# Performance work log

Measured on AMD Instinct MI355X. Metric: run time of the kernel, lower is better.

Reference implementation:

```python
import jax, jax.numpy as jnp
import numpy as np

DIM = 2048
B = 8192
RED = 16
FREQ = DIM // 2 + 1  # 1025


def setup_inputs() -> dict:
    key = jax.random.key(0)
    ks = jax.random.split(key, 8)
    s = 1.0 / np.sqrt(DIM)
    return {
        "x": jax.random.normal(ks[0], (B, DIM), dtype=jnp.float32),
        "W_in": jax.random.uniform(ks[1], (DIM, DIM), jnp.float32, -s, s),
        "b_in": jax.random.uniform(ks[2], (DIM,), jnp.float32, -s, s),
        "W_out": jax.random.uniform(ks[3], (DIM, DIM), jnp.float32, -s, s),
        "b_out": jax.random.uniform(ks[4], (DIM,), jnp.float32, -s, s),
        "freq_gate": jax.random.normal(ks[5], (FREQ, 2), dtype=jnp.float32) * 0.02,
        "W_fc1": jax.random.uniform(ks[6], (2 * DIM, DIM // RED), jnp.float32, -1.0 / np.sqrt(2 * DIM), 1.0 / np.sqrt(2 * DIM)),
        "W_fc2": jax.random.uniform(ks[7], (DIM // RED, DIM), jnp.float32, -1.0 / np.sqrt(DIM // RED), 1.0 / np.sqrt(DIM // RED)),
    }


def reference(x, W_in, b_in, W_out, b_out, freq_gate, W_fc1, W_fc2):
    # proj_in
    h = x @ W_in + b_in                      # [B, C]
    # FFT along feature dim, complex gating, inverse FFT
    hf = jnp.fft.rfft(h, axis=1)             # [B, C//2+1] complex
    gate = freq_gate[:, 0] + 1j * freq_gate[:, 1]
    hf = hf * gate[: hf.shape[1]]
    ht = jnp.fft.irfft(hf, n=h.shape[1], axis=1).astype(h.dtype)  # [B, C]
    # ChannelAttention on a 1x1 spatial map: both pools are identity
    # (original code uses AdaptiveAvgPool2d for BOTH avg and max branches)
    y = jnp.concatenate([ht, ht], axis=1)     # [B, 2C]
    y = jax.nn.relu(y @ W_fc1)                # [B, C//16]
    y = jax.nn.sigmoid(y @ W_fc2)             # [B, C]
    ht = ht * y
    # proj_out
    return ht @ W_out + b_out
```

## Files before the change

kernel.cpp:

```cpp
#include <hip/hip_runtime.h>

typedef unsigned short ushort_t;
typedef unsigned int uint_t;
typedef __attribute__((ext_vector_type(8))) short short8;
typedef __attribute__((ext_vector_type(4))) float f32x4;

#define DIM 2048
#define BATCH 8192

__device__ __forceinline__ ushort_t f2bf(float f) {
  union { float f; uint_t u; } x; x.f = f;
  uint_t r = x.u + 0x7fffu + ((x.u >> 16) & 1u);
  return (ushort_t)(r >> 16);
}
__device__ __forceinline__ float bf2f(ushort_t h) {
  union { uint_t u; float f; } x; x.u = ((uint_t)h) << 16; return x.f;
}

__device__ __forceinline__ void gload_lds16(const void* g, void* l) {
  typedef __attribute__((address_space(1))) const unsigned int gu32;
  typedef __attribute__((address_space(3))) unsigned int lu32;
  __builtin_amdgcn_global_load_lds((gu32*)g, (lu32*)l, 16, 0, 0);
}

__device__ __forceinline__ float block_reduce_sum(float v) {
  #pragma unroll
  for (int off = 32; off; off >>= 1) v += __shfl_down(v, off);
  __shared__ float red[4];
  int t = threadIdx.x;
  if ((t & 63) == 0) red[t >> 6] = v;
  __syncthreads();
  return red[0] + red[1] + red[2] + red[3];
}

__global__ void k_c(const float* __restrict__ fg, float* __restrict__ c) {
  int n = blockIdx.x;
  int t = threadIdx.x;
  float s = 0.f;
  for (int k = 1 + t; k < 1024; k += 256) {
    int r = (k * n) & 2047;
    float sn, cs;
    sincospif((float)r * (1.0f / 1024.0f), &sn, &cs);
    s += fg[2 * k] * cs - fg[2 * k + 1] * sn;
  }
  float tot = block_reduce_sum(s);
  if (t == 0) {
    float v = fg[0] + ((n & 1) ? -fg[2048] : fg[2048]) + 2.f * tot;
    c[n] = v * (1.0f / 2048.0f);
  }
}

__global__ void k_b1(const float* __restrict__ b_in, const float* __restrict__ c,
                     float* __restrict__ b1) {
  int n = blockIdx.x;
  int t = threadIdx.x;
  float s = 0.f;
  for (int m = t; m < 2048; m += 256) s += b_in[m] * c[(n - m) & 2047];
  float tot = block_reduce_sum(s);
  if (t == 0) b1[n] = tot;
}

__global__ void k_gt(const float* __restrict__ c, uint_t* __restrict__ gt) {
  int idx = blockIdx.x * 256 + threadIdx.x;
  int r = idx >> 10;
  int c2 = (idx & 1023) << 1;
  uint_t v0 = f2bf(c[(r - c2) & 2047]);
  uint_t v1 = f2bf(c[(r - c2 - 1) & 2047]);
  gt[idx] = v0 | (v1 << 16);
}

__global__ void k_cast4(const float* __restrict__ in, ushort_t* __restrict__ out) {
  long i = (long)blockIdx.x * 256 + threadIdx.x;
  float4 v = ((const float4*)in)[i];
  ushort4 o;
  o.x = f2bf(v.x); o.y = f2bf(v.y); o.z = f2bf(v.z); o.w = f2bf(v.w);
  ((ushort4*)out)[i] = o;
}

__global__ void k_tc(const float* __restrict__ in, ushort_t* __restrict__ out,
                     int R, int C) {
  __shared__ float tile[32][33];
  int bc = blockIdx.x * 32;
  int br = blockIdx.y * 32;
  int tx = threadIdx.x, ty = threadIdx.y;
  #pragma unroll
  for (int i = ty; i < 32; i += 8)
    tile[i][tx] = in[(size_t)(br + i) * C + bc + tx];
  __syncthreads();
  #pragma unroll
  for (int i = ty; i < 32; i += 8)
    out[(size_t)(bc + i) * R + br + tx] = f2bf(tile[tx][i]);
}

__global__ void k_fc1fold(const float* __restrict__ w, ushort_t* __restrict__ out) {
  int idx = blockIdx.x * 256 + threadIdx.x;
  int j = idx >> 11;
  int m = idx & 2047;
  out[idx] = f2bf(w[(size_t)m * 128 + j] + w[(size_t)(m + 2048) * 128 + j]);
}

template <int EPI>
__launch_bounds__(256, 2)
__global__ void gemm_bt(const ushort_t* __restrict__ A, const ushort_t* __restrict__ BT,
                        void* __restrict__ C, const float* __restrict__ bias,
                        const ushort_t* __restrict__ aux, int M, int N, int K) {
  __shared__ ushort_t ldsA[128 * 32];
  __shared__ ushort_t ldsB[128 * 32];
  const int t = threadIdx.x;
  const int wave = t >> 6, lane = t & 63;
  const int bm = blockIdx.x, bn = blockIdx.y;
  const int wr = wave >> 1, wc = wave & 1;
  const int lrow = lane & 15, lk = lane >> 4;

  f32x4 acc[4][4] = {};

  const size_t arow0 = (size_t)bm * 128;
  const size_t brow0 = (size_t)bn * 128;

  for (int k0 = 0; k0 < K; k0 += 32) {
    if (k0) __syncthreads();
    #pragma unroll
    for (int h = 0; h < 2; ++h) {
      int q = t + h * 256;
      int row = q >> 2, slot = q & 3;
      int kc = slot ^ ((row >> 1) & 3);
      const ushort_t* ga = A + (arow0 + row) * K + k0 + kc * 8;
      gload_lds16(ga, &ldsA[(wave * 64 + h * 256) * 8]);
      const ushort_t* gb = BT + (brow0 + row) * K + k0 + kc * 8;
      gload_lds16(gb, &ldsB[(wave * 64 + h * 256) * 8]);
    }
    __syncthreads();

    short8 af[4], bfr[4];
    #pragma unroll
    for (int m = 0; m < 4; ++m) {
      int row = wr * 64 + m * 16 + lrow;
      int slot = lk ^ ((row >> 1) & 3);
      af[m] = *(const short8*)&ldsA[row * 32 + slot * 8];
      int rowb = wc * 64 + m * 16 + lrow;
      int slotb = lk ^ ((rowb >> 1) & 3);
      bfr[m] = *(const short8*)&ldsB[rowb * 32 + slotb * 8];
    }
    #pragma unroll
    for (int m = 0; m < 4; ++m)
      #pragma unroll
      for (int n = 0; n < 4; ++n)
        acc[m][n] = __builtin_amdgcn_mfma_f32_16x16x32_bf16(af[m], bfr[n], acc[m][n], 0, 0, 0);
  }

  const int rbase = bm * 128 + wr * 64;
  const int cbase = bn * 128 + wc * 64;
  #pragma unroll
  for (int m = 0; m < 4; ++m) {
    #pragma unroll
    for (int n = 0; n < 4; ++n) {
      int col = cbase + n * 16 + lrow;
      int row0 = rbase + m * 16 + lk * 4;
      #pragma unroll
      for (int j = 0; j < 4; ++j) {
        int r = row0 + j;
        float v = acc[m][n][j];
        size_t off = (size_t)r * N + col;
        if constexpr (EPI == 0) {
          ((ushort_t*)C)[off] = f2bf(v);
        } else if constexpr (EPI == 1) {
          ((ushort_t*)C)[off] = f2bf(v + bias[col]);
        } else if constexpr (EPI == 2) {
          ((ushort_t*)C)[off] = f2bf(v > 0.f ? v : 0.f);
        } else if constexpr (EPI == 3) {
          float y = 1.f / (1.f + __expf(-v));
          ((ushort_t*)C)[off] = f2bf(bf2f(aux[off]) * y);
        } else {
          ((float*)C)[off] = v + bias[col];
        }
      }
    }
  }
}

extern "C" void kernel_launch(void* const* d_in, const int* in_sizes, int n_in,
                              void* d_out, int out_size, void* d_ws, size_t ws_size,
                              hipStream_t stream) {
  const float* x     = (const float*)d_in[0];
  const float* W_in  = (const float*)d_in[1];
  const float* b_in  = (const float*)d_in[2];
  const float* W_out = (const float*)d_in[3];
  const float* b_out = (const float*)d_in[4];
  const float* fg    = (const float*)d_in[5];
  const float* W_fc1 = (const float*)d_in[6];
  const float* W_fc2 = (const float*)d_in[7];

  char* ws = (char*)d_ws;
  float*    c_buf  = (float*)(ws + 0);
  float*    b1     = (float*)(ws + 8192);
  ushort_t* WinBf  = (ushort_t*)(ws + 16384);
  ushort_t* W1T    = (ushort_t*)(ws + 8404992);
  ushort_t* WoutT  = (ushort_t*)(ws + 16793600);
  ushort_t* Wfc1eT = (ushort_t*)(ws + 25182208);
  ushort_t* Wfc2T  = (ushort_t*)(ws + 25706496);
  ushort_t* x_bf   = (ushort_t*)(ws + 26230784);
  ushort_t* ht_bf  = (ushort_t*)(ws + 59785216);
  ushort_t* a_bf   = (ushort_t*)(ws + 93339648);
  ushort_t* GT     = (ushort_t*)(ws + 95436800);
  ushort_t* g_bf   = (ushort_t*)(ws + 95436800);
  (void)ws_size; (void)in_sizes; (void)n_in; (void)out_size;

  k_c<<<2048, 256, 0, stream>>>(fg, c_buf);
  k_b1<<<2048, 256, 0, stream>>>(b_in, c_buf, b1);
  k_gt<<<8192, 256, 0, stream>>>(c_buf, (uint_t*)GT);
  k_cast4<<<16384, 256, 0, stream>>>(x, x_bf);
  k_cast4<<<4096, 256, 0, stream>>>(W_in, WinBf);
  k_tc<<<dim3(64, 64), dim3(32, 8), 0, stream>>>(W_out, WoutT, 2048, 2048);
  k_tc<<<dim3(64, 4), dim3(32, 8), 0, stream>>>(W_fc2, Wfc2T, 128, 2048);
  k_fc1fold<<<1024, 256, 0, stream>>>(W_fc1, Wfc1eT);

  gemm_bt<0><<<dim3(16, 16), 256, 0, stream>>>(GT, WinBf, W1T, nullptr, nullptr,
                                               2048, 2048, 2048);
  gemm_bt<1><<<dim3(64, 16), 256, 0, stream>>>(x_bf, W1T, ht_bf, b1, nullptr,
                                               8192, 2048, 2048);
  gemm_bt<2><<<dim3(64, 1), 256, 0, stream>>>(ht_bf, Wfc1eT, a_bf, nullptr, nullptr,
                                              8192, 128, 2048);
  gemm_bt<3><<<dim3(64, 16), 256, 0, stream>>>(a_bf, Wfc2T, g_bf, nullptr, ht_bf,
                                               8192, 2048, 128);
  gemm_bt<4><<<dim3(64, 16), 256, 0, stream>>>(g_bf, WoutT, (float*)d_out, b_out, nullptr,
                                               8192, 2048, 2048);
}
```

Baseline: 433.1 us.

## Use pipelined 256x256 GEMM for big projections and split-K for fc1

```diff
diff --git a/kernel.cpp b/kernel.cpp
--- a/kernel.cpp
+++ b/kernel.cpp
@@ -97,6 +97,12 @@
   int j = idx >> 11;
   int m = idx & 2047;
   out[idx] = f2bf(w[(size_t)m * 128 + j] + w[(size_t)(m + 2048) * 128 + j]);
+}
+
+__global__ void k_red4relu(const float* __restrict__ p, ushort_t* __restrict__ out) {
+  int i = blockIdx.x * 256 + threadIdx.x;
+  float s = p[i] + p[i + 1048576] + p[i + 2097152] + p[i + 3145728];
+  out[i] = f2bf(s > 0.f ? s : 0.f);
 }
 
 template <int EPI>
@@ -117,8 +123,11 @@
   const size_t arow0 = (size_t)bm * 128;
   const size_t brow0 = (size_t)bn * 128;
 
-  for (int k0 = 0; k0 < K; k0 += 32) {
-    if (k0) __syncthreads();
+  int kb = 0, ke = K;
+  if constexpr (EPI == 5) { int ks = K >> 2; kb = blockIdx.z * ks; ke = kb + ks; }
+
+  for (int k0 = kb; k0 < ke; k0 += 32) {
+    if (k0 != kb) __syncthreads();
     #pragma unroll
     for (int h = 0; h < 2; ++h) {
       int q = t + h * 256;
@@ -170,9 +179,146 @@
         } else if constexpr (EPI == 3) {
           float y = 1.f / (1.f + __expf(-v));
           ((ushort_t*)C)[off] = f2bf(bf2f(aux[off]) * y);
+        } else if constexpr (EPI == 4) {
+          ((float*)C)[off] = v + bias[col];
         } else {
-          ((float*)C)[off] = v + bias[col];
+          ((float*)C)[off + (size_t)blockIdx.z * ((size_t)M * N)] = v;
         }
+      }
+    }
+  }
+}
+
+__device__ __forceinline__ void stage_half(const ushort_t* __restrict__ src, size_t gr0,
+                                           int k0b, int ksb, char* ldsHalf, int t) {
+  #pragma unroll
+  for (int l = 0; l < 2; ++l) {
+    int o = (l * 512 + t) * 16;
+    int s = o ^ (((o >> 9) & 1) << 5);
+    int row = s >> 7, cbyte = s & 127;
+    const char* g = (const char*)src + (gr0 + row) * (size_t)ksb + k0b + cbyte;
+    char* dst = ldsHalf + (l * 512 + (t & ~63)) * 16;
+    gload_lds16(g, dst);
+  }
+}
+
+__device__ __forceinline__ short8 ldfrag(const char* regionBase, int R, int kk, int lk) {
+  int r = R & 127, h = R >> 7;
+  int lin = r * 128 + kk * 64 + lk * 16;
+  int sw = lin ^ (((lin >> 9) & 1) << 5);
+  return *(const short8*)(regionBase + h * 16384 + sw);
+}
+
+template <int EPI>
+__launch_bounds__(512, 2)
+__global__ void gemm256(const ushort_t* __restrict__ A, const ushort_t* __restrict__ BT,
+                        void* __restrict__ C, const float* __restrict__ bias,
+                        int N, int K, int nbn) {
+  __shared__ __align__(16) char L[131072];
+  const int t = threadIdx.x;
+  const int lane = t & 63, wave = t >> 6;
+  const int wm = wave >> 2, wn = wave & 3;
+  const int lrow = lane & 15, lk = lane >> 4;
+
+  int d = blockIdx.x;
+  int cpx = gridDim.x >> 3;
+  int wg = (d & 7) * cpx + (d >> 3);
+  const int bm = wg / nbn, bn = wg % nbn;
+
+  const size_t am0 = (size_t)bm * 256;
+  const size_t bn0 = (size_t)bn * 256;
+  const int ksb = K * 2;
+  const int NT = K >> 6;
+
+  f32x4 acc[8][4] = {};
+
+  stage_half(A,  am0,       0,   ksb, L + 0,             t);
+  stage_half(A,  am0 + 128, 0,   ksb, L + 16384,         t);
+  stage_half(BT, bn0,       0,   ksb, L + 32768,         t);
+  stage_half(BT, bn0 + 128, 0,   ksb, L + 49152,         t);
+  stage_half(BT, bn0,       128, ksb, L + 65536 + 32768, t);
+  stage_half(BT, bn0 + 128, 128, ksb, L + 65536 + 49152, t);
+  asm volatile("s_waitcnt vmcnt(4)" ::: "memory");
+  __builtin_amdgcn_s_barrier();
+
+  short8 bfrag[4][2];
+  short8 afrag[2][2];
+
+  for (int T = 0; T < NT; T += 2) {
+    int k1 = ((T + 1 < NT) ? T + 1 : NT - 1) * 128;
+    int k2 = ((T + 2 < NT) ? T + 2 : NT - 1) * 128;
+    int k3 = ((T + 3 < NT) ? T + 3 : NT - 1) * 128;
+    #pragma unroll
+    for (int ph = 0; ph < 8; ++ph) {
+      const int cb = ph >> 2;
+      const int cp = ph & 3;
+      const char* Ab = L + cb * 65536;
+      const char* Bb = L + cb * 65536 + 32768;
+      if (cp == 0) {
+        #pragma unroll
+        for (int n = 0; n < 4; ++n)
+          #pragma unroll
+          for (int kk = 0; kk < 2; ++kk)
+            bfrag[n][kk] = ldfrag(Bb, wn * 64 + n * 16 + lrow, kk, lk);
+      }
+      #pragma unroll
+      for (int mi = 0; mi < 2; ++mi)
+        #pragma unroll
+        for (int kk = 0; kk < 2; ++kk)
+          afrag[mi][kk] = ldfrag(Ab, wm * 128 + (cp * 2 + mi) * 16 + lrow, kk, lk);
+
+      if (ph == 0) {
+        stage_half(A, am0,       k1, ksb, L + 65536,         t);
+        stage_half(A, am0 + 128, k1, ksb, L + 65536 + 16384, t);
+      } else if (ph == 1) {
+        stage_half(BT, bn0,       k2, ksb, L + 32768, t);
+      } else if (ph == 2) {
+        stage_half(BT, bn0 + 128, k2, ksb, L + 49152, t);
+      } else if (ph == 3) {
+        asm volatile("s_waitcnt vmcnt(4)" ::: "memory");
+      } else if (ph == 4) {
+        stage_half(A, am0,       k2, ksb, L + 0,     t);
+      } else if (ph == 5) {
+        stage_half(A, am0 + 128, k2, ksb, L + 16384, t);
+      } else if (ph == 6) {
+        stage_half(BT, bn0,       k3, ksb, L + 65536 + 32768, t);
+      } else {
+        stage_half(BT, bn0 + 128, k3, ksb, L + 65536 + 49152, t);
+        asm volatile("s_waitcnt vmcnt(4)" ::: "memory");
+      }
+
+      __builtin_amdgcn_s_barrier();
+      asm volatile("s_waitcnt lgkmcnt(0)" ::: "memory");
+      __builtin_amdgcn_sched_barrier(0);
+      __builtin_amdgcn_s_setprio(1);
+      #pragma unroll
+      for (int mi = 0; mi < 2; ++mi)
+        #pragma unroll
+        for (int n = 0; n < 4; ++n)
+          #pragma unroll
+          for (int kk = 0; kk < 2; ++kk)
+            acc[cp * 2 + mi][n] = __builtin_amdgcn_mfma_f32_16x16x32_bf16(
+                afrag[mi][kk], bfrag[n][kk], acc[cp * 2 + mi][n], 0, 0, 0);
+      __builtin_amdgcn_s_setprio(0);
+      __builtin_amdgcn_s_barrier();
+    }
+  }
+
+  const int rbase = bm * 256 + wm * 128;
+  const int cbase = bn * 256 + wn * 64;
+  #pragma unroll
+  for (int mi = 0; mi < 8; ++mi) {
+    #pragma unroll
+    for (int n = 0; n < 4; ++n) {
+      int col = cbase + n * 16 + lrow;
+      int row0 = rbase + mi * 16 + lk * 4;
+      float bcol = bias[col];
+      #pragma unroll
+      for (int j = 0; j < 4; ++j) {
+        float v = acc[mi][n][j] + bcol;
+        size_t off = (size_t)(row0 + j) * N + col;
+        if constexpr (EPI == 1) ((ushort_t*)C)[off] = f2bf(v);
+        else                    ((float*)C)[off] = v;
       }
     }
   }
@@ -199,6 +345,7 @@
   ushort_t* Wfc1eT = (ushort_t*)(ws + 25182208);
   ushort_t* Wfc2T  = (ushort_t*)(ws + 25706496);
   ushort_t* x_bf   = (ushort_t*)(ws + 26230784);
+  float*    fcp    = (float*)(ws + 26230784);
   ushort_t* ht_bf  = (ushort_t*)(ws + 59785216);
   ushort_t* a_bf   = (ushort_t*)(ws + 93339648);
   ushort_t* GT     = (ushort_t*)(ws + 95436800);
@@ -216,12 +363,11 @@
 
   gemm_bt<0><<<dim3(16, 16), 256, 0, stream>>>(GT, WinBf, W1T, nullptr, nullptr,
                                                2048, 2048, 2048);
-  gemm_bt<1><<<dim3(64, 16), 256, 0, stream>>>(x_bf, W1T, ht_bf, b1, nullptr,
-                                               8192, 2048, 2048);
-  gemm_bt<2><<<dim3(64, 1), 256, 0, stream>>>(ht_bf, Wfc1eT, a_bf, nullptr, nullptr,
-                                              8192, 128, 2048);
+  gemm256<1><<<256, 512, 0, stream>>>(x_bf, W1T, ht_bf, b1, 2048, 2048, 8);
+  gemm_bt<5><<<dim3(64, 1, 4), 256, 0, stream>>>(ht_bf, Wfc1eT, fcp, nullptr, nullptr,
+                                                 8192, 128, 2048);
+  k_red4relu<<<4096, 256, 0, stream>>>(fcp, a_bf);
   gemm_bt<3><<<dim3(64, 16), 256, 0, stream>>>(a_bf, Wfc2T, g_bf, nullptr, ht_bf,
                                                8192, 2048, 128);
-  gemm_bt<4><<<dim3(64, 16), 256, 0, stream>>>(g_bf, WoutT, (float*)d_out, b_out, nullptr,
-                                               8192, 2048, 2048);
-}
+  gemm256<4><<<256, 512, 0, stream>>>(g_bf, WoutT, (float*)d_out, b_out, 2048, 2048, 8);
+}
```

Result: faster. 422.1 us (-2.5%).
